# Kernel tuning notes

Hardware: AMD Instinct MI355X
Metric: run time of the kernel (lower is better)

The kernel has to match this reference:

```python
import jax, jax.numpy as jnp
import numpy as np

EMBED_DIM = 512

def setup_inputs() -> dict:
    key = jax.random.key(0)
    ks = jax.random.split(key, 5)
    D = EMBED_DIM
    x = jax.random.normal(ks[0], (4, 2048, D), dtype=jnp.float32)
    # qkv projection: weight [3D, D] (torch layout), bias [3D]
    qkv_w = jax.random.normal(ks[1], (3 * D, D), dtype=jnp.float32) * (D ** -0.5)
    qkv_b = jax.random.normal(ks[2], (3 * D,), dtype=jnp.float32) * 0.02
    out_w = jax.random.normal(ks[3], (D, D), dtype=jnp.float32) * (D ** -0.5)
    out_b = jax.random.normal(ks[4], (D,), dtype=jnp.float32) * 0.02
    return {"x": x, "qkv_w": qkv_w, "qkv_b": qkv_b, "out_w": out_w, "out_b": out_b}

def reference(x, qkv_w, qkv_b, out_w, out_b):
    D = x.shape[-1]
    scaling = D ** -0.5
    # qkv: [B, S, 3D]
    qkv = jnp.einsum('bsd,ed->bse', x, qkv_w) + qkv_b
    q, k, v = jnp.split(qkv, 3, axis=-1)
    q = q * scaling
    # scores: [B, S, S]
    attn = jnp.einsum('bqd,bkd->bqk', q, k)
    attn = jax.nn.softmax(attn, axis=-1)
    # dropout p=0.0 -> identity (eval-mode equivalent)
    out = jnp.einsum('bqk,bkd->bqd', attn, v)
    out = jnp.einsum('bsd,ed->bse', out, out_w) + out_b
    return out
```

## Files before the change

### kernel.cpp

```cpp
#include <hip/hip_runtime.h>

typedef _Float16 f16;
typedef _Float16 f16x2 __attribute__((ext_vector_type(2)));
typedef _Float16 f16x4 __attribute__((ext_vector_type(4)));
typedef _Float16 f16x8 __attribute__((ext_vector_type(8)));
typedef float f32x4 __attribute__((ext_vector_type(4)));
typedef float f32x16 __attribute__((ext_vector_type(16)));

#define MFMA16(a, b, c) __builtin_amdgcn_mfma_f32_16x16x32_f16((a), (b), (c), 0, 0, 0)
#define MFMA32(a, b, c) __builtin_amdgcn_mfma_f32_32x32x16_f16((a), (b), (c), 0, 0, 0)

__global__ void cvt_f32_f16(const float* __restrict__ s, f16* __restrict__ d, int n) {
    int i = (blockIdx.x * 256 + threadIdx.x) * 4;
    if (i < n) {
        float4 v = *(const float4*)(s + i);
        f16x4 o = {(f16)v.x, (f16)v.y, (f16)v.z, (f16)v.w};
        *(f16x4*)(d + i) = o;
    }
}

template<int MODE>
__global__ __launch_bounds__(256, 3) void gemm_nt(const f16* __restrict__ A, const f16* __restrict__ W,
                                                  const float* __restrict__ bias, float* __restrict__ Cf,
                                                  f16* __restrict__ Qb, f16* __restrict__ Kb,
                                                  f16* __restrict__ Vt) {
    __shared__ f16 As[2][128][40];
    __shared__ f16 Bs[2][128][40];
    const int m0 = blockIdx.x * 128, n0 = blockIdx.y * 128;
    const int tid = threadIdx.x;
    const int w = tid >> 6, l = tid & 63;
    const int wm = w >> 1, wn = w & 1;
    const int lr = l & 15, lg = l >> 4;
    const int srow = tid >> 1;
    const int scol = (tid & 1) * 16;
    const f16* ag = A + (size_t)(m0 + srow) * 512 + scol;
    const f16* bg = W + (size_t)(n0 + srow) * 512 + scol;
    f32x4 acc[4][4] = {};
    {
        f16x8 a0 = *(const f16x8*)(ag + 0), a1 = *(const f16x8*)(ag + 8);
        f16x8 b0 = *(const f16x8*)(bg + 0), b1 = *(const f16x8*)(bg + 8);
        *(f16x8*)&As[0][srow][scol] = a0;
        *(f16x8*)&As[0][srow][scol + 8] = a1;
        *(f16x8*)&Bs[0][srow][scol] = b0;
        *(f16x8*)&Bs[0][srow][scol + 8] = b1;
    }
    __syncthreads();
    int cur = 0;
    for (int k0 = 0; k0 < 512; k0 += 32) {
        f16x8 na0, na1, nb0, nb1;
        const bool more = (k0 + 32 < 512);
        if (more) {
            na0 = *(const f16x8*)(ag + k0 + 32);
            na1 = *(const f16x8*)(ag + k0 + 40);
            nb0 = *(const f16x8*)(bg + k0 + 32);
            nb1 = *(const f16x8*)(bg + k0 + 40);
        }
        f16x8 af[4], bf[4];
#pragma unroll
        for (int i = 0; i < 4; ++i) af[i] = *(f16x8*)&As[cur][64 * wm + 16 * i + lr][8 * lg];
#pragma unroll
        for (int i = 0; i < 4; ++i) bf[i] = *(f16x8*)&Bs[cur][64 * wn + 16 * i + lr][8 * lg];
#pragma unroll
        for (int mf = 0; mf < 4; ++mf)
#pragma unroll
            for (int nf = 0; nf < 4; ++nf) acc[mf][nf] = MFMA16(af[mf], bf[nf], acc[mf][nf]);
        if (more) {
            *(f16x8*)&As[cur ^ 1][srow][scol] = na0;
            *(f16x8*)&As[cur ^ 1][srow][scol + 8] = na1;
            *(f16x8*)&Bs[cur ^ 1][srow][scol] = nb0;
            *(f16x8*)&Bs[cur ^ 1][srow][scol + 8] = nb1;
            __syncthreads();
            cur ^= 1;
        }
    }
#pragma unroll
    for (int mf = 0; mf < 4; ++mf)
#pragma unroll
        for (int nf = 0; nf < 4; ++nf)
#pragma unroll
            for (int r = 0; r < 4; ++r) {
                int rr = 64 * wm + 16 * mf + 4 * lg + r;
                int cc = 64 * wn + 16 * nf + lr;
                int m = m0 + rr, e = n0 + cc;
                float val = acc[mf][nf][r] + bias[e];
                if (MODE == 0) {
                    int bb = m >> 11, s = m & 2047;
                    if (e < 512) {
                        Qb[((size_t)bb * 2048 + s) * 512 + e] = (f16)(val * 0.04419417382415922f);
                    } else if (e < 1024) {
                        int d = e - 512;
                        Kb[((((size_t)bb * 64 + (s >> 5)) * 32 + (d >> 4)) * 64
                            + ((d >> 3) & 1) * 32 + (s & 31)) * 8 + (d & 7)] = (f16)val;
                    } else {
                        int d = e - 1024;
                        Vt[((((size_t)bb * 16 + (d >> 5)) * 128 + (s >> 4)) * 64
                            + ((s >> 3) & 1) * 32 + (d & 31)) * 8 + (s & 7)] = (f16)val;
                    }
                } else {
                    Cf[(size_t)m * 512 + e] = val;
                }
            }
}

template<int NSPLIT, bool PART>
__global__ __launch_bounds__(512, 2) void flash_attn(const f16* __restrict__ Qb, const f16* __restrict__ Kb,
                                                     const f16* __restrict__ Vt, f16* __restrict__ AO,
                                                     f16* __restrict__ Opart, float* __restrict__ Ml) {
    __shared__ f16 Qs[32 * 512];
    __shared__ f16 P_lds[32 * 256];
    __shared__ float mbuf[32][8];
    __shared__ float lbuf[32][8];
    __shared__ float abuf[32];

    const int bid = blockIdx.x;
    const int xcd = bid & 7, slot = bid >> 3;
    const int b = xcd >> 1;
    const int t = slot * 2 + (xcd & 1);
    const int q0 = (t / NSPLIT) * 32;
    const int ks = t % NSPLIT;
    const int SPLITLEN = 2048 / NSPLIT;
    const int nkt = SPLITLEN / 256;

    const int tid = threadIdx.x;
    const int j = tid >> 6, l = tid & 63;
    const int q = l & 31, lh = l >> 5;

    const f16* Qg = Qb + ((size_t)b * 2048 + q0) * 512;
    const f16* Kg = Kb + ((size_t)b * 64 + (size_t)ks * (SPLITLEN / 32)) * 32 * 512;
    const f16* Vg = Vt + (size_t)b * 16 * 128 * 512 + (size_t)(ks * (SPLITLEN / 16)) * 512;

    for (int i = tid; i < 2048; i += 512) {
        int r = i >> 6, ch = i & 63;
        *(f16x8*)&Qs[r * 512 + ((ch ^ (r & 7)) * 8)] = *(const f16x8*)&Qg[(size_t)r * 512 + ch * 8];
    }

    f32x16 o[2] = {};
    float m_st = -1e30f, l_st = 0.f;
    char* Pq = (char*)&P_lds[0];
    const uint swz = ((uint)(q & 15)) << 4;
    const int qbase = q * 512, qx = q & 7;
    __syncthreads();

    for (int kt = 0; kt < nkt; ++kt) {
        const int key0 = kt * 256;
        const f16* kp = Kg + ((size_t)((key0 >> 5) + j) * 32) * 512 + (size_t)l * 8;
        const f16* vpb = Vg + ((size_t)(2 * j) * 128 + (key0 >> 4)) * 512 + (size_t)l * 8;
        f16x8 kr[8], vr[8];
#pragma unroll
        for (int i = 0; i < 8; ++i) kr[i] = *(const f16x8*)(kp + (size_t)i * 512);
#pragma unroll
        for (int i = 0; i < 4; ++i) {
            vr[2 * i] = *(const f16x8*)(vpb + (size_t)i * 512);
            vr[2 * i + 1] = *(const f16x8*)(vpb + (size_t)(128 + i) * 512);
        }
        f32x16 sA = {}, sB = {};
#pragma unroll
        for (int kc = 0; kc < 32; kc += 2) {
            f16x8 k0 = kr[kc & 7];
            f16x8 k1 = kr[(kc & 7) + 1];
            if (kc < 24) {
                kr[kc & 7] = *(const f16x8*)(kp + (size_t)(kc + 8) * 512);
                kr[(kc & 7) + 1] = *(const f16x8*)(kp + (size_t)(kc + 9) * 512);
            }
            f16x8 q0f = *(f16x8*)&Qs[qbase + (((2 * kc + lh) ^ qx) * 8)];
            f16x8 q1f = *(f16x8*)&Qs[qbase + (((2 * kc + 2 + lh) ^ qx) * 8)];
            sA = MFMA32(k0, q0f, sA);
            sB = MFMA32(k1, q1f, sB);
        }
        float s[16];
#pragma unroll
        for (int r = 0; r < 16; ++r) s[r] = sA[r] + sB[r];
        float mt = s[0];
#pragma unroll
        for (int r = 1; r < 16; ++r) mt = fmaxf(mt, s[r]);
        mt = fmaxf(mt, __shfl_xor(mt, 32));
        if (l < 32) mbuf[q][j] = mt;
        __syncthreads();
        float mnew = m_st;
        {
            float4 mv0 = *(float4*)&mbuf[q][0];
            float4 mv1 = *(float4*)&mbuf[q][4];
            mnew = fmaxf(mnew, fmaxf(fmaxf(mv0.x, mv0.y), fmaxf(mv0.z, mv0.w)));
            mnew = fmaxf(mnew, fmaxf(fmaxf(mv1.x, mv1.y), fmaxf(mv1.z, mv1.w)));
        }
        float alpha = __expf(m_st - mnew);
        if (l < 32) abuf[q] = alpha;
        float ps = 0.f;
#pragma unroll
        for (int r = 0; r < 16; ++r) {
            s[r] = __expf(s[r] - mnew);
            ps += s[r];
        }
        ps += __shfl_xor(ps, 32);
        if (l < 32) lbuf[q][j] = ps;
        {
            const uint rowb = (uint)q * 512;
#pragma unroll
            for (int i = 0; i < 4; ++i) {
                int key = 8 * i + 4 * lh + 32 * j;
                f16x4 pk = {(f16)s[4 * i], (f16)s[4 * i + 1], (f16)s[4 * i + 2], (f16)s[4 * i + 3]};
                *(f16x4*)(Pq + ((rowb + (uint)key * 2) ^ swz)) = pk;
            }
        }
        m_st = mnew;
        __syncthreads();
        {
            float4 lv0 = *(float4*)&lbuf[q][0];
            float4 lv1 = *(float4*)&lbuf[q][4];
            l_st = l_st * alpha + ((lv0.x + lv0.y) + (lv0.z + lv0.w))
                                + ((lv1.x + lv1.y) + (lv1.z + lv1.w));
        }
        float av[4][4];
#pragma unroll
        for (int g = 0; g < 4; ++g) {
            float4 a4 = *(float4*)&abuf[8 * g + 4 * lh];
            av[g][0] = a4.x; av[g][1] = a4.y; av[g][2] = a4.z; av[g][3] = a4.w;
        }
#pragma unroll
        for (int dt = 0; dt < 2; ++dt)
#pragma unroll
            for (int r = 0; r < 16; ++r) o[dt][r] *= av[r >> 2][r & 3];
#pragma unroll
        for (int kk = 0; kk < 16; ++kk) {
            f16x8 v0 = vr[(kk & 3) * 2];
            f16x8 v1 = vr[(kk & 3) * 2 + 1];
            if (kk < 12) {
                vr[(kk & 3) * 2] = *(const f16x8*)(vpb + (size_t)(kk + 4) * 512);
                vr[(kk & 3) * 2 + 1] = *(const f16x8*)(vpb + (size_t)(128 + kk + 4) * 512);
            }
            f16x8 paf = *(f16x8*)(Pq + (((uint)q * 512 + (uint)(16 * kk + 8 * lh) * 2) ^ swz));
            o[0] = MFMA32(paf, v0, o[0]);
            o[1] = MFMA32(paf, v1, o[1]);
        }
    }
    __syncthreads();
    if (l < 32) abuf[q] = l_st;
    if (PART && l < 32 && j == 0) {
        Ml[((size_t)bid * 32 + q) * 2 + 0] = m_st;
        Ml[((size_t)bid * 32 + q) * 2 + 1] = l_st;
    }
    __syncthreads();
    float iv[4][4];
#pragma unroll
    for (int g = 0; g < 4; ++g) {
        float4 a4 = *(float4*)&abuf[8 * g + 4 * lh];
        iv[g][0] = 1.f / a4.x; iv[g][1] = 1.f / a4.y; iv[g][2] = 1.f / a4.z; iv[g][3] = 1.f / a4.w;
    }
    f16* op = PART ? (Opart + (size_t)bid * 32 * 512 + 64 * j)
                   : (AO + ((size_t)(b * 2048 + q0)) * 512 + 64 * j);
#pragma unroll
    for (int r = 0; r < 16; ++r) {
        int qr = (r & 3) + 8 * (r >> 2) + 4 * lh;
        float inv = iv[r >> 2][r & 3];
#pragma unroll
        for (int dt = 0; dt < 2; ++dt)
            op[(size_t)qr * 512 + 32 * dt + q] = (f16)(o[dt][r] * inv);
    }
}

template<int NS>
__global__ __launch_bounds__(256) void combineN(const f16* __restrict__ Opart, const float* __restrict__ Ml,
                                                f16* __restrict__ AO) {
    int gid = blockIdx.x * 256 + threadIdx.x;
    int row = gid >> 6, col0 = (gid & 63) * 8;
    int b = row >> 11, qq = row & 2047;
    int qb = qq >> 5, qr = qq & 31;
    int bids[NS];
    float m[NS], ll[NS];
#pragma unroll
    for (int s = 0; s < NS; ++s) {
        int t = qb * NS + s;
        bids[s] = (t >> 1) * 8 + 2 * b + (t & 1);
        m[s] = Ml[((size_t)bids[s] * 32 + qr) * 2];
        ll[s] = Ml[((size_t)bids[s] * 32 + qr) * 2 + 1];
    }
    float M = m[0];
#pragma unroll
    for (int s = 1; s < NS; ++s) M = fmaxf(M, m[s]);
    float c[NS], W = 0.f;
#pragma unroll
    for (int s = 0; s < NS; ++s) {
        c[s] = __expf(m[s] - M) * ll[s];
        W += c[s];
    }
    float invW = 1.f / W;
    float av[8] = {};
#pragma unroll
    for (int s = 0; s < NS; ++s) {
        f16x8 v = *(const f16x8*)&Opart[((size_t)bids[s] * 32 + qr) * 512 + col0];
        float cs = c[s] * invW;
#pragma unroll
        for (int jj = 0; jj < 8; ++jj) av[jj] += cs * (float)v[jj];
    }
    f16x8 o8;
#pragma unroll
    for (int jj = 0; jj < 8; ++jj) o8[jj] = (f16)av[jj];
    *(f16x8*)&AO[(size_t)row * 512 + col0] = o8;
}

extern "C" void kernel_launch(void* const* d_in, const int* in_sizes, int n_in,
                              void* d_out, int out_size, void* d_ws, size_t ws_size,
                              hipStream_t stream) {
    (void)in_sizes; (void)n_in; (void)out_size;
    const float* x = (const float*)d_in[0];
    const float* qkv_w = (const float*)d_in[1];
    const float* qkv_b = (const float*)d_in[2];
    const float* out_w = (const float*)d_in[3];
    const float* out_b = (const float*)d_in[4];
    char* ws = (char*)d_ws;
    f16* xh    = (f16*)(ws + 0);
    f16* wqkvh = (f16*)(ws + 8388608);
    f16* wouth = (f16*)(ws + 9961472);
    f16* Qb    = (f16*)(ws + 10485760);
    f16* Kb    = (f16*)(ws + 18874368);
    f16* Vt    = (f16*)(ws + 27262976);
    f16* AO    = (f16*)(ws + 35651584);
    f16* Opart = (f16*)(ws + 44040192);
    float* Ml  = (float*)(ws + 44040192 + 16777216);
    const size_t NEED = 44040192ull + 16777216ull + 131072ull;

    cvt_f32_f16<<<4096, 256, 0, stream>>>(x, xh, 4194304);
    cvt_f32_f16<<<768, 256, 0, stream>>>(qkv_w, wqkvh, 786432);
    cvt_f32_f16<<<256, 256, 0, stream>>>(out_w, wouth, 262144);

    gemm_nt<0><<<dim3(64, 12), 256, 0, stream>>>(xh, wqkvh, qkv_b, nullptr, Qb, Kb, Vt);

    if (ws_size >= NEED) {
        flash_attn<2, true><<<512, 512, 0, stream>>>(Qb, Kb, Vt, nullptr, Opart, Ml);
        combineN<2><<<2048, 256, 0, stream>>>(Opart, Ml, AO);
    } else {
        flash_attn<1, false><<<256, 512, 0, stream>>>(Qb, Kb, Vt, AO, nullptr, nullptr);
    }

    gemm_nt<1><<<dim3(64, 4), 256, 0, stream>>>(AO, wouth, out_b, (float*)d_out,
                                                nullptr, nullptr, nullptr);
}
```

Before: 118.7 us.

## Use direct global-to-LDS loads in GEMM, prefetch K, drop split-KV attention

The GEMM now stages tiles with global_load_lds straight into an unpadded LDS layout, replacing the register round-trip, and raises wave priority around the MFMA blocks. Flash attention drops the 2-way KV split and its combine kernel, so 256 blocks each process the full key range. The next K tile is prefetched into registers during the softmax phase. The unpadded LDS layout may add bank conflicts, and halving the attention grid lowers parallelism in exchange for removing the combine pass and partial-output traffic.

```diff
diff --git a/kernel.cpp b/kernel.cpp
--- a/kernel.cpp
+++ b/kernel.cpp
@@ -10,6 +10,9 @@
 #define MFMA16(a, b, c) __builtin_amdgcn_mfma_f32_16x16x32_f16((a), (b), (c), 0, 0, 0)
 #define MFMA32(a, b, c) __builtin_amdgcn_mfma_f32_32x32x16_f16((a), (b), (c), 0, 0, 0)
 
+typedef const __attribute__((address_space(1))) void gv_t;
+typedef __attribute__((address_space(3))) void lv_t;
+
 __global__ void cvt_f32_f16(const float* __restrict__ s, f16* __restrict__ d, int n) {
     int i = (blockIdx.x * 256 + threadIdx.x) * 4;
     if (i < n) {
@@ -24,54 +27,56 @@
                                                   const float* __restrict__ bias, float* __restrict__ Cf,
                                                   f16* __restrict__ Qb, f16* __restrict__ Kb,
                                                   f16* __restrict__ Vt) {
-    __shared__ f16 As[2][128][40];
-    __shared__ f16 Bs[2][128][40];
+    __shared__ f16 As[2][128 * 32];
+    __shared__ f16 Bs[2][128 * 32];
     const int m0 = blockIdx.x * 128, n0 = blockIdx.y * 128;
     const int tid = threadIdx.x;
     const int w = tid >> 6, l = tid & 63;
     const int wm = w >> 1, wn = w & 1;
     const int lr = l & 15, lg = l >> 4;
-    const int srow = tid >> 1;
-    const int scol = (tid & 1) * 16;
-    const f16* ag = A + (size_t)(m0 + srow) * 512 + scol;
-    const f16* bg = W + (size_t)(n0 + srow) * 512 + scol;
+    const int R = w * 16 + (l >> 2);
+    const int ldsoff = w * 512;
+    const int lidx = ldsoff + l * 8;
+    const f16* ag = A + (size_t)(m0 + R) * 512 + (l & 3) * 8;
+    const f16* bg = W + (size_t)(n0 + R) * 512 + (l & 3) * 8;
+    (void)lidx;
+
+#if __has_builtin(__builtin_amdgcn_global_load_lds)
+#define GLDS(gp, lp) __builtin_amdgcn_global_load_lds((gv_t*)(gp), (lv_t*)(lp), 16, 0, 0)
+#define STAGE(k0, buf) do {                                   \
+        GLDS(ag + (k0), &As[buf][ldsoff]);                    \
+        GLDS(ag + 64 * 512 + (k0), &As[buf][ldsoff + 2048]);  \
+        GLDS(bg + (k0), &Bs[buf][ldsoff]);                    \
+        GLDS(bg + 64 * 512 + (k0), &Bs[buf][ldsoff + 2048]);  \
+    } while (0)
+#else
+#define STAGE(k0, buf) do {                                                      \
+        *(f16x8*)&As[buf][lidx] = *(const f16x8*)(ag + (k0));                    \
+        *(f16x8*)&As[buf][lidx + 2048] = *(const f16x8*)(ag + 64 * 512 + (k0));  \
+        *(f16x8*)&Bs[buf][lidx] = *(const f16x8*)(bg + (k0));                    \
+        *(f16x8*)&Bs[buf][lidx + 2048] = *(const f16x8*)(bg + 64 * 512 + (k0));  \
+    } while (0)
+#endif
+
     f32x4 acc[4][4] = {};
-    {
-        f16x8 a0 = *(const f16x8*)(ag + 0), a1 = *(const f16x8*)(ag + 8);
-        f16x8 b0 = *(const f16x8*)(bg + 0), b1 = *(const f16x8*)(bg + 8);
-        *(f16x8*)&As[0][srow][scol] = a0;
-        *(f16x8*)&As[0][srow][scol + 8] = a1;
-        *(f16x8*)&Bs[0][srow][scol] = b0;
-        *(f16x8*)&Bs[0][srow][scol + 8] = b1;
-    }
+    STAGE(0, 0);
     __syncthreads();
     int cur = 0;
     for (int k0 = 0; k0 < 512; k0 += 32) {
-        f16x8 na0, na1, nb0, nb1;
-        const bool more = (k0 + 32 < 512);
-        if (more) {
-            na0 = *(const f16x8*)(ag + k0 + 32);
-            na1 = *(const f16x8*)(ag + k0 + 40);
-            nb0 = *(const f16x8*)(bg + k0 + 32);
-            nb1 = *(const f16x8*)(bg + k0 + 40);
-        }
+        if (k0 + 32 < 512) STAGE(k0 + 32, cur ^ 1);
         f16x8 af[4], bf[4];
 #pragma unroll
-        for (int i = 0; i < 4; ++i) af[i] = *(f16x8*)&As[cur][64 * wm + 16 * i + lr][8 * lg];
-#pragma unroll
-        for (int i = 0; i < 4; ++i) bf[i] = *(f16x8*)&Bs[cur][64 * wn + 16 * i + lr][8 * lg];
+        for (int i = 0; i < 4; ++i) af[i] = *(f16x8*)&As[cur][(64 * wm + 16 * i + lr) * 32 + lg * 8];
+#pragma unroll
+        for (int i = 0; i < 4; ++i) bf[i] = *(f16x8*)&Bs[cur][(64 * wn + 16 * i + lr) * 32 + lg * 8];
+        __builtin_amdgcn_s_setprio(1);
 #pragma unroll
         for (int mf = 0; mf < 4; ++mf)
 #pragma unroll
             for (int nf = 0; nf < 4; ++nf) acc[mf][nf] = MFMA16(af[mf], bf[nf], acc[mf][nf]);
-        if (more) {
-            *(f16x8*)&As[cur ^ 1][srow][scol] = na0;
-            *(f16x8*)&As[cur ^ 1][srow][scol + 8] = na1;
-            *(f16x8*)&Bs[cur ^ 1][srow][scol] = nb0;
-            *(f16x8*)&Bs[cur ^ 1][srow][scol + 8] = nb1;
-            __syncthreads();
-            cur ^= 1;
-        }
+        __builtin_amdgcn_s_setprio(0);
+        __syncthreads();
+        cur ^= 1;
     }
 #pragma unroll
     for (int mf = 0; mf < 4; ++mf)
@@ -100,12 +105,11 @@
                     Cf[(size_t)m * 512 + e] = val;
                 }
             }
-}
-
-template<int NSPLIT, bool PART>
+#undef STAGE
+}
+
 __global__ __launch_bounds__(512, 2) void flash_attn(const f16* __restrict__ Qb, const f16* __restrict__ Kb,
-                                                     const f16* __restrict__ Vt, f16* __restrict__ AO,
-                                                     f16* __restrict__ Opart, float* __restrict__ Ml) {
+                                                     const f16* __restrict__ Vt, f16* __restrict__ AO) {
     __shared__ f16 Qs[32 * 512];
     __shared__ f16 P_lds[32 * 256];
     __shared__ float mbuf[32][8];
@@ -116,18 +120,16 @@
     const int xcd = bid & 7, slot = bid >> 3;
     const int b = xcd >> 1;
     const int t = slot * 2 + (xcd & 1);
-    const int q0 = (t / NSPLIT) * 32;
-    const int ks = t % NSPLIT;
-    const int SPLITLEN = 2048 / NSPLIT;
-    const int nkt = SPLITLEN / 256;
+    const int q0 = t * 32;
+    const int nkt = 8;
 
     const int tid = threadIdx.x;
     const int j = tid >> 6, l = tid & 63;
     const int q = l & 31, lh = l >> 5;
 
     const f16* Qg = Qb + ((size_t)b * 2048 + q0) * 512;
-    const f16* Kg = Kb + ((size_t)b * 64 + (size_t)ks * (SPLITLEN / 32)) * 32 * 512;
-    const f16* Vg = Vt + (size_t)b * 16 * 128 * 512 + (size_t)(ks * (SPLITLEN / 16)) * 512;
+    const f16* Kg = Kb + (size_t)b * 64 * 32 * 512;
+    const f16* Vg = Vt + (size_t)b * 16 * 128 * 512;
 
     for (int i = tid; i < 2048; i += 512) {
         int r = i >> 6, ch = i & 63;
@@ -139,21 +141,25 @@
     char* Pq = (char*)&P_lds[0];
     const uint swz = ((uint)(q & 15)) << 4;
     const int qbase = q * 512, qx = q & 7;
+    f16x8 kr[8], vr[8];
+    {
+        const f16* kp0 = Kg + (size_t)j * 32 * 512 + (size_t)l * 8;
+#pragma unroll
+        for (int i = 0; i < 8; ++i) kr[i] = *(const f16x8*)(kp0 + (size_t)i * 512);
+    }
     __syncthreads();
 
     for (int kt = 0; kt < nkt; ++kt) {
         const int key0 = kt * 256;
         const f16* kp = Kg + ((size_t)((key0 >> 5) + j) * 32) * 512 + (size_t)l * 8;
         const f16* vpb = Vg + ((size_t)(2 * j) * 128 + (key0 >> 4)) * 512 + (size_t)l * 8;
-        f16x8 kr[8], vr[8];
-#pragma unroll
-        for (int i = 0; i < 8; ++i) kr[i] = *(const f16x8*)(kp + (size_t)i * 512);
 #pragma unroll
         for (int i = 0; i < 4; ++i) {
             vr[2 * i] = *(const f16x8*)(vpb + (size_t)i * 512);
             vr[2 * i + 1] = *(const f16x8*)(vpb + (size_t)(128 + i) * 512);
         }
         f32x16 sA = {}, sB = {};
+        __builtin_amdgcn_s_setprio(1);
 #pragma unroll
         for (int kc = 0; kc < 32; kc += 2) {
             f16x8 k0 = kr[kc & 7];
@@ -167,6 +173,7 @@
             sA = MFMA32(k0, q0f, sA);
             sB = MFMA32(k1, q1f, sB);
         }
+        __builtin_amdgcn_s_setprio(0);
         float s[16];
 #pragma unroll
         for (int r = 0; r < 16; ++r) s[r] = sA[r] + sB[r];
@@ -204,6 +211,11 @@
         }
         m_st = mnew;
         __syncthreads();
+        if (kt + 1 < nkt) {
+            const f16* kpn = Kg + ((size_t)(((key0 + 256) >> 5) + j) * 32) * 512 + (size_t)l * 8;
+#pragma unroll
+            for (int i = 0; i < 8; ++i) kr[i] = *(const f16x8*)(kpn + (size_t)i * 512);
+        }
         {
             float4 lv0 = *(float4*)&lbuf[q][0];
             float4 lv1 = *(float4*)&lbuf[q][4];
@@ -220,6 +232,7 @@
         for (int dt = 0; dt < 2; ++dt)
 #pragma unroll
             for (int r = 0; r < 16; ++r) o[dt][r] *= av[r >> 2][r & 3];
+        __builtin_amdgcn_s_setprio(1);
 #pragma unroll
         for (int kk = 0; kk < 16; ++kk) {
             f16x8 v0 = vr[(kk & 3) * 2];
@@ -232,13 +245,10 @@
             o[0] = MFMA32(paf, v0, o[0]);
             o[1] = MFMA32(paf, v1, o[1]);
         }
+        __builtin_amdgcn_s_setprio(0);
     }
     __syncthreads();
     if (l < 32) abuf[q] = l_st;
-    if (PART && l < 32 && j == 0) {
-        Ml[((size_t)bid * 32 + q) * 2 + 0] = m_st;
-        Ml[((size_t)bid * 32 + q) * 2 + 1] = l_st;
-    }
     __syncthreads();
     float iv[4][4];
 #pragma unroll
@@ -246,8 +256,7 @@
         float4 a4 = *(float4*)&abuf[8 * g + 4 * lh];
         iv[g][0] = 1.f / a4.x; iv[g][1] = 1.f / a4.y; iv[g][2] = 1.f / a4.z; iv[g][3] = 1.f / a4.w;
     }
-    f16* op = PART ? (Opart + (size_t)bid * 32 * 512 + 64 * j)
-                   : (AO + ((size_t)(b * 2048 + q0)) * 512 + 64 * j);
+    f16* op = AO + ((size_t)(b * 2048 + q0)) * 512 + 64 * j;
 #pragma unroll
     for (int r = 0; r < 16; ++r) {
         int qr = (r & 3) + 8 * (r >> 2) + 4 * lh;
@@ -258,50 +267,10 @@
     }
 }
 
-template<int NS>
-__global__ __launch_bounds__(256) void combineN(const f16* __restrict__ Opart, const float* __restrict__ Ml,
-                                                f16* __restrict__ AO) {
-    int gid = blockIdx.x * 256 + threadIdx.x;
-    int row = gid >> 6, col0 = (gid & 63) * 8;
-    int b = row >> 11, qq = row & 2047;
-    int qb = qq >> 5, qr = qq & 31;
-    int bids[NS];
-    float m[NS], ll[NS];
-#pragma unroll
-    for (int s = 0; s < NS; ++s) {
-        int t = qb * NS + s;
-        bids[s] = (t >> 1) * 8 + 2 * b + (t & 1);
-        m[s] = Ml[((size_t)bids[s] * 32 + qr) * 2];
-        ll[s] = Ml[((size_t)bids[s] * 32 + qr) * 2 + 1];
-    }
-    float M = m[0];
-#pragma unroll
-    for (int s = 1; s < NS; ++s) M = fmaxf(M, m[s]);
-    float c[NS], W = 0.f;
-#pragma unroll
-    for (int s = 0; s < NS; ++s) {
-        c[s] = __expf(m[s] - M) * ll[s];
-        W += c[s];
-    }
-    float invW = 1.f / W;
-    float av[8] = {};
-#pragma unroll
-    for (int s = 0; s < NS; ++s) {
-        f16x8 v = *(const f16x8*)&Opart[((size_t)bids[s] * 32 + qr) * 512 + col0];
-        float cs = c[s] * invW;
-#pragma unroll
-        for (int jj = 0; jj < 8; ++jj) av[jj] += cs * (float)v[jj];
-    }
-    f16x8 o8;
-#pragma unroll
-    for (int jj = 0; jj < 8; ++jj) o8[jj] = (f16)av[jj];
-    *(f16x8*)&AO[(size_t)row * 512 + col0] = o8;
-}
-
 extern "C" void kernel_launch(void* const* d_in, const int* in_sizes, int n_in,
                               void* d_out, int out_size, void* d_ws, size_t ws_size,
                               hipStream_t stream) {
-    (void)in_sizes; (void)n_in; (void)out_size;
+    (void)in_sizes; (void)n_in; (void)out_size; (void)ws_size;
     const float* x = (const float*)d_in[0];
     const float* qkv_w = (const float*)d_in[1];
     const float* qkv_b = (const float*)d_in[2];
@@ -315,9 +284,6 @@
     f16* Kb    = (f16*)(ws + 18874368);
     f16* Vt    = (f16*)(ws + 27262976);
     f16* AO    = (f16*)(ws + 35651584);
-    f16* Opart = (f16*)(ws + 44040192);
-    float* Ml  = (float*)(ws + 44040192 + 16777216);
-    const size_t NEED = 44040192ull + 16777216ull + 131072ull;
 
     cvt_f32_f16<<<4096, 256, 0, stream>>>(x, xh, 4194304);
     cvt_f32_f16<<<768, 256, 0, stream>>>(qkv_w, wqkvh, 786432);
@@ -325,12 +291,7 @@
 
     gemm_nt<0><<<dim3(64, 12), 256, 0, stream>>>(xh, wqkvh, qkv_b, nullptr, Qb, Kb, Vt);
 
-    if (ws_size >= NEED) {
-        flash_attn<2, true><<<512, 512, 0, stream>>>(Qb, Kb, Vt, nullptr, Opart, Ml);
-        combineN<2><<<2048, 256, 0, stream>>>(Opart, Ml, AO);
-    } else {
-        flash_attn<1, false><<<256, 512, 0, stream>>>(Qb, Kb, Vt, AO, nullptr, nullptr);
-    }
+    flash_attn<<<256, 512, 0, stream>>>(Qb, Kb, Vt, AO);
 
     gemm_nt<1><<<dim3(64, 4), 256, 0, stream>>>(AO, wouth, out_b, (float*)d_out,
                                                 nullptr, nullptr, nullptr);
```

New measurement: 121.9 us. +2.7%, slower.

## Merge conversion kernels, use global_load_lds in GEMM, prefetch K tiles in attention

Applied to the files above, without the earlier changes.

Merges the three f32-to-f16 conversion launches into one kernel that writes a contiguous workspace region. The GEMM now stages tiles through direct global-to-LDS loads when the builtin is available, dropping the padded LDS layout and register staging. Attention keeps 16 K fragments in registers and prefetches the next tile's K during the softmax phase. s_setprio is raised around the MFMA loops. The unpadded LDS layout risks bank conflicts on the fragment reads, and the larger K register buffer may raise register pressure.

```diff
diff --git a/kernel.cpp b/kernel.cpp
--- a/kernel.cpp
+++ b/kernel.cpp
@@ -10,13 +10,20 @@
 #define MFMA16(a, b, c) __builtin_amdgcn_mfma_f32_16x16x32_f16((a), (b), (c), 0, 0, 0)
 #define MFMA32(a, b, c) __builtin_amdgcn_mfma_f32_32x32x16_f16((a), (b), (c), 0, 0, 0)
 
-__global__ void cvt_f32_f16(const float* __restrict__ s, f16* __restrict__ d, int n) {
+typedef const __attribute__((address_space(1))) void gv_t;
+typedef __attribute__((address_space(3))) void lv_t;
+
+__global__ void cvt_all(const float* __restrict__ x, const float* __restrict__ qw,
+                        const float* __restrict__ ow, f16* __restrict__ d) {
     int i = (blockIdx.x * 256 + threadIdx.x) * 4;
-    if (i < n) {
-        float4 v = *(const float4*)(s + i);
-        f16x4 o = {(f16)v.x, (f16)v.y, (f16)v.z, (f16)v.w};
-        *(f16x4*)(d + i) = o;
-    }
+    const float* s;
+    int off;
+    if (i < 4194304) { s = x; off = i; }
+    else if (i < 4980736) { s = qw; off = i - 4194304; }
+    else { s = ow; off = i - 4980736; }
+    float4 v = *(const float4*)(s + off);
+    f16x4 o = {(f16)v.x, (f16)v.y, (f16)v.z, (f16)v.w};
+    *(f16x4*)(d + i) = o;
 }
 
 template<int MODE>
@@ -24,54 +31,56 @@
                                                   const float* __restrict__ bias, float* __restrict__ Cf,
                                                   f16* __restrict__ Qb, f16* __restrict__ Kb,
                                                   f16* __restrict__ Vt) {
-    __shared__ f16 As[2][128][40];
-    __shared__ f16 Bs[2][128][40];
+    __shared__ f16 As[2][128 * 32];
+    __shared__ f16 Bs[2][128 * 32];
     const int m0 = blockIdx.x * 128, n0 = blockIdx.y * 128;
     const int tid = threadIdx.x;
     const int w = tid >> 6, l = tid & 63;
     const int wm = w >> 1, wn = w & 1;
     const int lr = l & 15, lg = l >> 4;
-    const int srow = tid >> 1;
-    const int scol = (tid & 1) * 16;
-    const f16* ag = A + (size_t)(m0 + srow) * 512 + scol;
-    const f16* bg = W + (size_t)(n0 + srow) * 512 + scol;
+    const int R = w * 16 + (l >> 2);
+    const int ldsoff = w * 512;
+    const int lidx = ldsoff + l * 8;
+    const f16* ag = A + (size_t)(m0 + R) * 512 + (l & 3) * 8;
+    const f16* bg = W + (size_t)(n0 + R) * 512 + (l & 3) * 8;
+    (void)lidx;
+
+#if __has_builtin(__builtin_amdgcn_global_load_lds)
+#define GLDS(gp, lp) __builtin_amdgcn_global_load_lds((gv_t*)(gp), (lv_t*)(lp), 16, 0, 0)
+#define STAGE(k0, buf) do {                                   \
+        GLDS(ag + (k0), &As[buf][ldsoff]);                    \
+        GLDS(ag + 64 * 512 + (k0), &As[buf][ldsoff + 2048]);  \
+        GLDS(bg + (k0), &Bs[buf][ldsoff]);                    \
+        GLDS(bg + 64 * 512 + (k0), &Bs[buf][ldsoff + 2048]);  \
+    } while (0)
+#else
+#define STAGE(k0, buf) do {                                                      \
+        *(f16x8*)&As[buf][lidx] = *(const f16x8*)(ag + (k0));                    \
+        *(f16x8*)&As[buf][lidx + 2048] = *(const f16x8*)(ag + 64 * 512 + (k0));  \
+        *(f16x8*)&Bs[buf][lidx] = *(const f16x8*)(bg + (k0));                    \
+        *(f16x8*)&Bs[buf][lidx + 2048] = *(const f16x8*)(bg + 64 * 512 + (k0));  \
+    } while (0)
+#endif
+
     f32x4 acc[4][4] = {};
-    {
-        f16x8 a0 = *(const f16x8*)(ag + 0), a1 = *(const f16x8*)(ag + 8);
-        f16x8 b0 = *(const f16x8*)(bg + 0), b1 = *(const f16x8*)(bg + 8);
-        *(f16x8*)&As[0][srow][scol] = a0;
-        *(f16x8*)&As[0][srow][scol + 8] = a1;
-        *(f16x8*)&Bs[0][srow][scol] = b0;
-        *(f16x8*)&Bs[0][srow][scol + 8] = b1;
-    }
+    STAGE(0, 0);
     __syncthreads();
     int cur = 0;
     for (int k0 = 0; k0 < 512; k0 += 32) {
-        f16x8 na0, na1, nb0, nb1;
-        const bool more = (k0 + 32 < 512);
-        if (more) {
-            na0 = *(const f16x8*)(ag + k0 + 32);
-            na1 = *(const f16x8*)(ag + k0 + 40);
-            nb0 = *(const f16x8*)(bg + k0 + 32);
-            nb1 = *(const f16x8*)(bg + k0 + 40);
-        }
+        if (k0 + 32 < 512) STAGE(k0 + 32, cur ^ 1);
         f16x8 af[4], bf[4];
 #pragma unroll
-        for (int i = 0; i < 4; ++i) af[i] = *(f16x8*)&As[cur][64 * wm + 16 * i + lr][8 * lg];
-#pragma unroll
-        for (int i = 0; i < 4; ++i) bf[i] = *(f16x8*)&Bs[cur][64 * wn + 16 * i + lr][8 * lg];
+        for (int i = 0; i < 4; ++i) af[i] = *(f16x8*)&As[cur][(64 * wm + 16 * i + lr) * 32 + lg * 8];
+#pragma unroll
+        for (int i = 0; i < 4; ++i) bf[i] = *(f16x8*)&Bs[cur][(64 * wn + 16 * i + lr) * 32 + lg * 8];
+        __builtin_amdgcn_s_setprio(1);
 #pragma unroll
         for (int mf = 0; mf < 4; ++mf)
 #pragma unroll
             for (int nf = 0; nf < 4; ++nf) acc[mf][nf] = MFMA16(af[mf], bf[nf], acc[mf][nf]);
-        if (more) {
-            *(f16x8*)&As[cur ^ 1][srow][scol] = na0;
-            *(f16x8*)&As[cur ^ 1][srow][scol + 8] = na1;
-            *(f16x8*)&Bs[cur ^ 1][srow][scol] = nb0;
-            *(f16x8*)&Bs[cur ^ 1][srow][scol + 8] = nb1;
-            __syncthreads();
-            cur ^= 1;
-        }
+        __builtin_amdgcn_s_setprio(0);
+        __syncthreads();
+        cur ^= 1;
     }
 #pragma unroll
     for (int mf = 0; mf < 4; ++mf)
@@ -100,6 +109,7 @@
                     Cf[(size_t)m * 512 + e] = val;
                 }
             }
+#undef STAGE
 }
 
 template<int NSPLIT, bool PART>
@@ -139,34 +149,39 @@
     char* Pq = (char*)&P_lds[0];
     const uint swz = ((uint)(q & 15)) << 4;
     const int qbase = q * 512, qx = q & 7;
+    f16x8 kr[16], vr[8];
+    {
+        const f16* kp0 = Kg + (size_t)j * 32 * 512 + (size_t)l * 8;
+#pragma unroll
+        for (int i = 0; i < 16; ++i) kr[i] = *(const f16x8*)(kp0 + (size_t)i * 512);
+    }
     __syncthreads();
 
     for (int kt = 0; kt < nkt; ++kt) {
         const int key0 = kt * 256;
         const f16* kp = Kg + ((size_t)((key0 >> 5) + j) * 32) * 512 + (size_t)l * 8;
         const f16* vpb = Vg + ((size_t)(2 * j) * 128 + (key0 >> 4)) * 512 + (size_t)l * 8;
-        f16x8 kr[8], vr[8];
-#pragma unroll
-        for (int i = 0; i < 8; ++i) kr[i] = *(const f16x8*)(kp + (size_t)i * 512);
 #pragma unroll
         for (int i = 0; i < 4; ++i) {
             vr[2 * i] = *(const f16x8*)(vpb + (size_t)i * 512);
             vr[2 * i + 1] = *(const f16x8*)(vpb + (size_t)(128 + i) * 512);
         }
         f32x16 sA = {}, sB = {};
+        __builtin_amdgcn_s_setprio(1);
 #pragma unroll
         for (int kc = 0; kc < 32; kc += 2) {
-            f16x8 k0 = kr[kc & 7];
-            f16x8 k1 = kr[(kc & 7) + 1];
-            if (kc < 24) {
-                kr[kc & 7] = *(const f16x8*)(kp + (size_t)(kc + 8) * 512);
-                kr[(kc & 7) + 1] = *(const f16x8*)(kp + (size_t)(kc + 9) * 512);
+            f16x8 k0 = kr[kc & 15];
+            f16x8 k1 = kr[(kc & 15) + 1];
+            if (kc < 16) {
+                kr[kc] = *(const f16x8*)(kp + (size_t)(kc + 16) * 512);
+                kr[kc + 1] = *(const f16x8*)(kp + (size_t)(kc + 17) * 512);
             }
             f16x8 q0f = *(f16x8*)&Qs[qbase + (((2 * kc + lh) ^ qx) * 8)];
             f16x8 q1f = *(f16x8*)&Qs[qbase + (((2 * kc + 2 + lh) ^ qx) * 8)];
             sA = MFMA32(k0, q0f, sA);
             sB = MFMA32(k1, q1f, sB);
         }
+        __builtin_amdgcn_s_setprio(0);
         float s[16];
 #pragma unroll
         for (int r = 0; r < 16; ++r) s[r] = sA[r] + sB[r];
@@ -204,6 +219,11 @@
         }
         m_st = mnew;
         __syncthreads();
+        if (kt + 1 < nkt) {
+            const f16* kpn = Kg + ((size_t)(((key0 + 256) >> 5) + j) * 32) * 512 + (size_t)l * 8;
+#pragma unroll
+            for (int i = 0; i < 16; ++i) kr[i] = *(const f16x8*)(kpn + (size_t)i * 512);
+        }
         {
             float4 lv0 = *(float4*)&lbuf[q][0];
             float4 lv1 = *(float4*)&lbuf[q][4];
@@ -220,6 +240,7 @@
         for (int dt = 0; dt < 2; ++dt)
 #pragma unroll
             for (int r = 0; r < 16; ++r) o[dt][r] *= av[r >> 2][r & 3];
+        __builtin_amdgcn_s_setprio(1);
 #pragma unroll
         for (int kk = 0; kk < 16; ++kk) {
             f16x8 v0 = vr[(kk & 3) * 2];
@@ -232,6 +253,7 @@
             o[0] = MFMA32(paf, v0, o[0]);
             o[1] = MFMA32(paf, v1, o[1]);
         }
+        __builtin_amdgcn_s_setprio(0);
     }
     __syncthreads();
     if (l < 32) abuf[q] = l_st;
@@ -318,10 +340,9 @@
     f16* Opart = (f16*)(ws + 44040192);
     float* Ml  = (float*)(ws + 44040192 + 16777216);
     const size_t NEED = 44040192ull + 16777216ull + 131072ull;
-
-    cvt_f32_f16<<<4096, 256, 0, stream>>>(x, xh, 4194304);
-    cvt_f32_f16<<<768, 256, 0, stream>>>(qkv_w, wqkvh, 786432);
-    cvt_f32_f16<<<256, 256, 0, stream>>>(out_w, wouth, 262144);
+    (void)wqkvh; (void)wouth;
+
+    cvt_all<<<5120, 256, 0, stream>>>(x, qkv_w, out_w, xh);
 
     gemm_nt<0><<<dim3(64, 12), 256, 0, stream>>>(xh, wqkvh, qkv_b, nullptr, Qb, Kb, Vt);
 
```

Measured after the change: 118.0 us. About the same (-0.6%).
